# Performance work log

Hardware: AMD Instinct MI355X
Metric: run time of the kernel (lower is better)

Reference implementation:

```python
import jax, jax.numpy as jnp
import numpy as np

B, S, H, NH, HD, I = 2, 1024, 4096, 32, 128, 11008
EPS = 1e-6
THETA = 10000.0


def _rmsnorm(x, w):
    v = jnp.mean(x * x, axis=-1, keepdims=True)
    return x * jax.lax.rsqrt(v + EPS) * w


def _quant(x):
    # per-tensor symmetric int8 quantization (scale already folded upstream)
    return jnp.clip(jnp.round(x), -128.0, 127.0)


def _lin_i8(xq_i8, w_i8, scale, bias):
    acc = jnp.matmul(xq_i8.astype(jnp.int32), w_i8.astype(jnp.int32).T)
    return acc.astype(jnp.float32) * scale + bias


def _rope(q, k):
    pos = jnp.arange(S, dtype=jnp.float32)
    inv = 1.0 / (THETA ** (jnp.arange(0, HD, 2, dtype=jnp.float32) / HD))
    f = pos[:, None] * inv[None, :]              # [S, HD/2]
    emb = jnp.concatenate([f, f], axis=-1)        # [S, HD]
    cos = jnp.cos(emb)[None, None]                # [1,1,S,HD]
    sin = jnp.sin(emb)[None, None]
    def rot(x):
        return jnp.concatenate([-x[..., HD // 2:], x[..., :HD // 2]], axis=-1)
    return q * cos + rot(q) * sin, k * cos + rot(k) * sin


def setup_inputs() -> dict:
    key = jax.random.key(0)
    ks = jax.random.split(key, 30)
    def w8(k, o, i):
        return jax.random.randint(k, (o, i), -128, 128, dtype=jnp.int8)
    def sc(k):
        return jax.random.uniform(k, (), jnp.float32, 0.001, 0.01)
    return {
        "hidden_states": jax.random.normal(ks[0], (B, S, H), jnp.float32),
        "ln1_w": jax.random.uniform(ks[1], (H,), jnp.float32, 0.5, 1.5) * 20.0,
        "ln2_w": jax.random.uniform(ks[2], (H,), jnp.float32, 0.5, 1.5) * 20.0,
        "Wq": w8(ks[3], H, H), "Wk": w8(ks[4], H, H), "Wv": w8(ks[5], H, H),
        "Wo": w8(ks[6], H, H),
        "Wg": w8(ks[7], I, H), "Wu": w8(ks[8], I, H), "Wd": w8(ks[9], H, I),
        "bq": jax.random.normal(ks[10], (H,), jnp.float32) * 0.01,
        "bk": jax.random.normal(ks[11], (H,), jnp.float32) * 0.01,
        "bv": jax.random.normal(ks[12], (H,), jnp.float32) * 0.01,
        "bo": jax.random.normal(ks[13], (H,), jnp.float32) * 0.01,
        "bg": jax.random.normal(ks[14], (I,), jnp.float32) * 0.01,
        "bu": jax.random.normal(ks[15], (I,), jnp.float32) * 0.01,
        "bd": jax.random.normal(ks[16], (H,), jnp.float32) * 0.01,
        "sq": sc(ks[17]) * 1e-3, "sk": sc(ks[18]) * 1e-3, "sv": sc(ks[19]) * 1e-3,
        "so": sc(ks[20]) * 1e-3, "sg": sc(ks[21]) * 1e-3, "su": sc(ks[22]) * 1e-3,
        "sd": sc(ks[23]) * 1e-3,
        "o_in_scale": sc(ks[24]), "down_in_scale": sc(ks[25]),
    }


def reference(hidden_states, ln1_w, ln2_w, Wq, Wk, Wv, Wo, Wg, Wu, Wd,
              bq, bk, bv, bo, bg, bu, bd,
              sq, sk, sv, so, sg, su, sd, o_in_scale, down_in_scale):
    residual = hidden_states
    # input RMSNorm (quant scale folded into ln1_w) -> int8 activation
    hq = _quant(_rmsnorm(hidden_states, ln1_w)).astype(jnp.int8)
    q = _lin_i8(hq, Wq, sq, bq).reshape(B, S, NH, HD).transpose(0, 2, 1, 3)
    k = _lin_i8(hq, Wk, sk, bk).reshape(B, S, NH, HD).transpose(0, 2, 1, 3)
    v = _lin_i8(hq, Wv, sv, bv).reshape(B, S, NH, HD).transpose(0, 2, 1, 3)
    q, k = _rope(q, k)
    scores = jnp.einsum("bhqd,bhkd->bhqk", q, k) / np.float32(np.sqrt(HD))
    causal = jnp.tril(jnp.ones((S, S), dtype=bool))
    scores = jnp.where(causal[None, None], scores, jnp.float32(-1e30))
    attn = jax.nn.softmax(scores, axis=-1)
    o = jnp.einsum("bhqk,bhkd->bhqd", attn, v).transpose(0, 2, 1, 3).reshape(B, S, H)
    # o_proj with quant scale (W8A8BFP32OFP32LinearWithQuantScale)
    oq = _quant(o / o_in_scale).astype(jnp.int8)
    h = residual + _lin_i8(oq, Wo, so, bo)
    residual = h
    # post-attention RMSNorm (fc1 quant scale folded into ln2_w)
    hq2 = _quant(_rmsnorm(h, ln2_w)).astype(jnp.int8)
    g = _lin_i8(hq2, Wg, sg, bg)
    u = _lin_i8(hq2, Wu, su, bu)
    a = jax.nn.silu(g) * u
    aq = _quant(a / down_in_scale).astype(jnp.int8)
    out = residual + _lin_i8(aq, Wd, sd, bd)
    return out
```

## Files before the change

kernel.cpp:

```cpp
#include <hip/hip_runtime.h>
#include <math.h>

#define B_  2
#define S_  1024
#define H_  4096
#define NH_ 32
#define HD_ 128
#define I_  11008
#define R_  2048

typedef __attribute__((ext_vector_type(4))) int i32x4;
typedef __attribute__((ext_vector_type(4))) float f32x4;
typedef __attribute__((ext_vector_type(8))) short bf16x8;


__device__ __forceinline__ void gload_lds16(const void* g, void* l) {
    __builtin_amdgcn_global_load_lds(
        (const __attribute__((address_space(1))) unsigned int*)g,
        (__attribute__((address_space(3))) unsigned int*)l, 16, 0, 0);
}

__device__ __forceinline__ unsigned short f2bf(float f) {
    unsigned int u = __float_as_uint(f);
    u += 0x7fffu + ((u >> 16) & 1u);
    return (unsigned short)(u >> 16);
}

__global__ __launch_bounds__(256)
void packW_k(const int* __restrict__ W, signed char* __restrict__ out, const int K)
{
    const int kt = blockIdx.x, cb = blockIdx.y, nk = gridDim.x;
    const int t = threadIdx.x;
    int* otile = (int*)(out + ((long)(cb * nk + kt) << 13));
#pragma unroll
    for (int i = 0; i < 8; ++i) {
        const int o = i * 256 + t;
        const int g = o >> 9, r = (o >> 2) & 127, jj = o & 3;
        const int4 w4 = *(const int4*)(W + (long)(cb * 128 + r) * K + kt * 64 + g * 16 + jj * 4);
        otile[o] = (w4.x & 255) | ((w4.y & 255) << 8) | ((w4.z & 255) << 16) | (w4.w << 24);
    }
}

__global__ __launch_bounds__(256)
void rmsnorm_quant_k(const float* __restrict__ x, const float* __restrict__ w,
                     signed char* __restrict__ out)
{
    __shared__ float red[4];
    const int tid = threadIdx.x;
    const long row = blockIdx.x;
    const float4* xr = (const float4*)(x + row * H_);
    float4 xv[4];
    float ss = 0.f;
#pragma unroll
    for (int i = 0; i < 4; ++i) {
        xv[i] = xr[tid + i * 256];
        ss += xv[i].x * xv[i].x + xv[i].y * xv[i].y
            + xv[i].z * xv[i].z + xv[i].w * xv[i].w;
    }
#pragma unroll
    for (int off = 32; off; off >>= 1) ss += __shfl_xor(ss, off);
    if ((tid & 63) == 0) red[tid >> 6] = ss;
    __syncthreads();
    const float tot = red[0] + red[1] + red[2] + red[3];
    const float sc = 1.f / sqrtf(tot * (1.f / (float)H_) + 1e-6f);
    const float4* wr = (const float4*)w;
    int* ob = (int*)out;
    const long rb = row >> 7;
    const int rr = (int)(row & 127);
#pragma unroll
    for (int i = 0; i < 4; ++i) {
        const float4 wv = wr[tid + i * 256];
        const int b0 = (int)fminf(fmaxf(rintf(xv[i].x * sc * wv.x), -128.f), 127.f);
        const int b1 = (int)fminf(fmaxf(rintf(xv[i].y * sc * wv.y), -128.f), 127.f);
        const int b2 = (int)fminf(fmaxf(rintf(xv[i].z * sc * wv.z), -128.f), 127.f);
        const int b3 = (int)fminf(fmaxf(rintf(xv[i].w * sc * wv.w), -128.f), 127.f);
        const int packed = (b0 & 255) | ((b1 & 255) << 8) | ((b2 & 255) << 16) | (b3 << 24);
        const int j4 = tid + i * 256;
        const long a32 = ((rb * 64 + (j4 >> 4)) << 11) + (((j4 >> 2) & 3) << 9)
                       + (rr << 2) + (j4 & 3);
        ob[a32] = packed;
    }
}

template<int MODE>
__global__ __launch_bounds__(256, 4)
void gemm_i8t(const signed char* __restrict__ A8, const signed char* __restrict__ W8,
              const float* __restrict__ scale_ptr, const float* __restrict__ bias,
              const float* __restrict__ residual, float* __restrict__ C,
              const float* __restrict__ gbuf, const float* __restrict__ qscale,
              signed char* __restrict__ out8,
              const int N, const int K, const int gx)
{
    __shared__ __align__(16) signed char lsA[2][8192];
    __shared__ __align__(16) signed char lsB[2][8192];

    int bid = blockIdx.x;
    {
        const int nwg = gridDim.x;
        const int q = nwg >> 3, r = nwg & 7;
        const int xcd = bid & 7, idx = bid >> 3;
        bid = (xcd < r) ? (xcd * (q + 1) + idx)
                        : (r * (q + 1) + (xcd - r) * q + idx);
    }
    const int bx = bid % gx, by = bid / gx;

    const int tid  = threadIdx.x;
    const int lane = tid & 63, wid = tid >> 6;
    const int bm = bx << 7, bn = by << 7;
    const int wm = (wid >> 1) << 6, wn = (wid & 1) << 6;

    i32x4 acc[4][4];
#pragma unroll
    for (int m = 0; m < 4; ++m)
#pragma unroll
        for (int n = 0; n < 4; ++n) acc[m][n] = (i32x4){0, 0, 0, 0};

    const int nk = K >> 6;
    const signed char* abase = A8 + ((long)bx * nk << 13);
    const signed char* bbase = W8 + ((long)by * nk << 13);
    const int so0 = wid * 2048 + lane * 16;

    {
        const signed char* at = abase;
        const signed char* bt = bbase;
        gload_lds16(at + so0,        lsA[0] + wid * 2048);
        gload_lds16(at + so0 + 1024, lsA[0] + wid * 2048 + 1024);
        gload_lds16(bt + so0,        lsB[0] + wid * 2048);
        gload_lds16(bt + so0 + 1024, lsB[0] + wid * 2048 + 1024);
    }
    __syncthreads();

    int cur = 0;
    for (int kt = 0; kt < nk; ++kt) {
        const int nxt = cur ^ 1;
        if (kt + 1 < nk) {
            const signed char* at = abase + ((long)(kt + 1) << 13);
            const signed char* bt = bbase + ((long)(kt + 1) << 13);
            gload_lds16(at + so0,        lsA[nxt] + wid * 2048);
            gload_lds16(at + so0 + 1024, lsA[nxt] + wid * 2048 + 1024);
            gload_lds16(bt + so0,        lsB[nxt] + wid * 2048);
            gload_lds16(bt + so0 + 1024, lsB[nxt] + wid * 2048 + 1024);
        }

        const int kg = (lane >> 4) * 2048, fr = (lane & 15) * 16;
        i32x4 af[4], bf[4];
#pragma unroll
        for (int m = 0; m < 4; ++m)
            af[m] = *(const i32x4*)(lsA[cur] + kg + wm * 16 + m * 256 + fr);
#pragma unroll
        for (int n = 0; n < 4; ++n)
            bf[n] = *(const i32x4*)(lsB[cur] + kg + wn * 16 + n * 256 + fr);
#pragma unroll
        for (int m = 0; m < 4; ++m)
#pragma unroll
            for (int n = 0; n < 4; ++n)
                acc[m][n] = __builtin_amdgcn_mfma_i32_16x16x64_i8(af[m], bf[n], acc[m][n], 0, 0, 0);

        __syncthreads();
        cur = nxt;
    }

    const float s = *scale_ptr;
    const int rq = (lane >> 4) * 4, fc = lane & 15;
    if (MODE == 0) {
#pragma unroll
        for (int m = 0; m < 4; ++m) {
#pragma unroll
            for (int n = 0; n < 4; ++n) {
                const int col = bn + wn + n * 16 + fc;
                const float bcol = bias[col];
#pragma unroll
                for (int r = 0; r < 4; ++r) {
                    const int row = bm + wm + m * 16 + rq + r;
                    float v = (float)acc[m][n][r] * s + bcol;
                    if (residual) v += residual[(long)row * N + col];
                    C[(long)row * N + col] = v;
                }
            }
        }
    } else {
        const float dinv = 1.f / qscale[0];
        const int nko = N >> 6;
#pragma unroll
        for (int m = 0; m < 4; ++m) {
#pragma unroll
            for (int n = 0; n < 4; ++n) {
                const int col = bn + wn + n * 16 + fc;
                const float bcol = bias[col];
                const int ktc = col >> 6, kgc = (col >> 4) & 3, jc = col & 15;
#pragma unroll
                for (int r = 0; r < 4; ++r) {
                    const int row = bm + wm + m * 16 + rq + r;
                    const float u = (float)acc[m][n][r] * s + bcol;
                    const float g = gbuf[(long)row * N + col];
                    const float a = g / (1.f + __expf(-g)) * u;
                    const float qv = fminf(fmaxf(rintf(a * dinv), -128.f), 127.f);
                    const long addr = (((long)(row >> 7) * nko + ktc) << 13)
                                    + (kgc << 11) + ((row & 127) << 4) + jc;
                    out8[addr] = (signed char)(int)qv;
                }
            }
        }
    }
}

__global__ __launch_bounds__(256)
void rope_k(float* __restrict__ q, float* __restrict__ k)
{
    const int row = blockIdx.x;
    const int s = row & (S_ - 1);
    float* qr = q + (long)row * H_;
    float* kr = k + (long)row * H_;
    for (int t = threadIdx.x; t < NH_ * 64; t += 256) {
        const int nh = t >> 6, i = t & 63;
        const float inv = powf(10000.f, -(float)(2 * i) * (1.f / 128.f));
        const float f = (float)s * inv;
        float sn, c;
        sincosf(f, &sn, &c);
        const int base = nh * 128 + i;
        const float q0 = qr[base], q1 = qr[base + 64];
        qr[base]      = q0 * c - q1 * sn;
        qr[base + 64] = q1 * c + q0 * sn;
        const float k0 = kr[base], k1 = kr[base + 64];
        kr[base]      = k0 * c - k1 * sn;
        kr[base + 64] = k1 * c + k0 * sn;
    }
}

__global__ __launch_bounds__(256, 2)
void attn_mfma_k(const float* __restrict__ q, const float* __restrict__ k,
                 const float* __restrict__ v, signed char* __restrict__ out8,
                 const float* __restrict__ osc)
{
    __shared__ __align__(16) char lsK[8192];
    __shared__ __align__(16) char lsV[10240];
    __shared__ __align__(16) char lsP[4][1024];

    const int tid = threadIdx.x, lane = tid & 63, wid = tid >> 6;
    const int bid = blockIdx.x;
    const int qt = 15 - (bid >> 6);
    const int bh = bid & 63;
    const int b = bh >> 5, h = bh & 31;
    const int q0 = qt * 64;
    const int qw = q0 + wid * 16;

    const float* qbase = q + (long)(b * S_) * H_ + (long)h * HD_;
    const float* kbase = k + (long)(b * S_) * H_ + (long)h * HD_;
    const float* vbase = v + (long)(b * S_) * H_ + (long)h * HD_;

    const int frow = lane & 15, fgrp = lane >> 4;
    const float sc = 0.08838834764831845f;

    bf16x8 qf[4];
    {
        const float* qr = qbase + (long)(qw + frow) * H_;
#pragma unroll
        for (int c = 0; c < 4; ++c) {
            const float4 a = *(const float4*)(qr + c * 32 + fgrp * 8);
            const float4 bq = *(const float4*)(qr + c * 32 + fgrp * 8 + 4);
            bf16x8 t;
            t[0] = (short)f2bf(a.x * sc);  t[1] = (short)f2bf(a.y * sc);
            t[2] = (short)f2bf(a.z * sc);  t[3] = (short)f2bf(a.w * sc);
            t[4] = (short)f2bf(bq.x * sc); t[5] = (short)f2bf(bq.y * sc);
            t[6] = (short)f2bf(bq.z * sc); t[7] = (short)f2bf(bq.w * sc);
            qf[c] = t;
        }
    }

    f32x4 oacc[8];
#pragma unroll
    for (int n2 = 0; n2 < 8; ++n2) oacc[n2] = (f32x4){0.f, 0.f, 0.f, 0.f};
    float mr[4] = {-1e30f, -1e30f, -1e30f, -1e30f};
    float lr[4] = {0.f, 0.f, 0.f, 0.f};

    const int nt = (q0 >> 5) + 2;
    for (int kt = 0; kt < nt; ++kt) {
        if (kt) __syncthreads();
        {
            const float* kg = kbase + (long)(kt * 32) * H_;
            const float* vg = vbase + (long)(kt * 32) * H_;
#pragma unroll
            for (int i = 0; i < 4; ++i) {
                const int lin = i * 256 + tid;
                const int kr = lin >> 5;
                const int d4 = (lin & 31) * 4;
                const float4 kv = *(const float4*)(kg + (long)kr * H_ + d4);
                const float4 vv = *(const float4*)(vg + (long)kr * H_ + d4);
                ushort4 kb;
                kb.x = f2bf(kv.x); kb.y = f2bf(kv.y); kb.z = f2bf(kv.z); kb.w = f2bf(kv.w);
                *(ushort4*)(lsK + kr * 256 + ((d4 * 2) ^ ((kr & 7) << 4))) = kb;
                *(unsigned short*)(lsV + (d4 + 0) * 80 + kr * 2) = f2bf(vv.x);
                *(unsigned short*)(lsV + (d4 + 1) * 80 + kr * 2) = f2bf(vv.y);
                *(unsigned short*)(lsV + (d4 + 2) * 80 + kr * 2) = f2bf(vv.z);
                *(unsigned short*)(lsV + (d4 + 3) * 80 + kr * 2) = f2bf(vv.w);
            }
        }
        __syncthreads();

        if (kt * 32 <= qw + 15) {
            f32x4 s0 = (f32x4){0.f, 0.f, 0.f, 0.f};
            f32x4 s1 = (f32x4){0.f, 0.f, 0.f, 0.f};
            const int swz = (frow & 7) << 4;
#pragma unroll
            for (int c = 0; c < 4; ++c) {
                const int dby = c * 64 + fgrp * 16;
                const bf16x8 kfA = *(const bf16x8*)(lsK + frow * 256 + (dby ^ swz));
                const bf16x8 kfB = *(const bf16x8*)(lsK + (frow + 16) * 256 + (dby ^ swz));
                s0 = __builtin_amdgcn_mfma_f32_16x16x32_bf16(qf[c], kfA, s0, 0, 0, 0);
                s1 = __builtin_amdgcn_mfma_f32_16x16x32_bf16(qf[c], kfB, s1, 0, 0, 0);
            }

            const int colg0 = kt * 32 + frow;
            float cf[4];
#pragma unroll
            for (int r = 0; r < 4; ++r) {
                const int rowg = qw + fgrp * 4 + r;
                const float a0 = (colg0 <= rowg) ? s0[r] : -1e30f;
                const float a1 = (colg0 + 16 <= rowg) ? s1[r] : -1e30f;
                float mx = fmaxf(a0, a1);
#pragma unroll
                for (int off2 = 1; off2 < 16; off2 <<= 1) mx = fmaxf(mx, __shfl_xor(mx, off2));
                const float mnew = fmaxf(mr[r], mx);
                cf[r] = __expf(mr[r] - mnew);
                mr[r] = mnew;
                const float p0 = __expf(a0 - mnew);
                const float p1 = __expf(a1 - mnew);
                float sm = p0 + p1;
#pragma unroll
                for (int off2 = 1; off2 < 16; off2 <<= 1) sm += __shfl_xor(sm, off2);
                lr[r] = lr[r] * cf[r] + sm;
                const int row = fgrp * 4 + r;
                const int psw = (row & 3) << 4;
                *(unsigned short*)(lsP[wid] + row * 64 + ((frow * 2) ^ psw)) = f2bf(p0);
                *(unsigned short*)(lsP[wid] + row * 64 + (((16 + frow) * 2) ^ psw)) = f2bf(p1);
            }
#pragma unroll
            for (int n2 = 0; n2 < 8; ++n2) {
#pragma unroll
                for (int r = 0; r < 4; ++r) oacc[n2][r] *= cf[r];
            }
            const bf16x8 pf = *(const bf16x8*)(lsP[wid] + frow * 64 + ((fgrp * 16) ^ ((frow & 3) << 4)));
#pragma unroll
            for (int n2 = 0; n2 < 8; ++n2) {
                const bf16x8 vf = *(const bf16x8*)(lsV + (n2 * 16 + frow) * 80 + fgrp * 16);
                oacc[n2] = __builtin_amdgcn_mfma_f32_16x16x32_bf16(pf, vf, oacc[n2], 0, 0, 0);
            }
        }
    }

    const float oinv = 1.f / osc[0];
    float inv[4];
#pragma unroll
    for (int r = 0; r < 4; ++r) inv[r] = 1.f / lr[r];
#pragma unroll
    for (int n2 = 0; n2 < 8; ++n2) {
        const int kk = h * 128 + n2 * 16 + frow;
        const int ktc = kk >> 6, kgc = (kk >> 4) & 3, jc = kk & 15;
#pragma unroll
        for (int r = 0; r < 4; ++r) {
            const int rowt = b * S_ + qw + fgrp * 4 + r;
            const float ov = oacc[n2][r] * inv[r];
            const float qv = fminf(fmaxf(rintf(ov * oinv), -128.f), 127.f);
            const long addr = (((long)(rowt >> 7) * 64 + ktc) << 13)
                            + (kgc << 11) + ((rowt & 127) << 4) + jc;
            out8[addr] = (signed char)(int)qv;
        }
    }
}

extern "C" void kernel_launch(void* const* d_in, const int* in_sizes, int n_in,
                              void* d_out, int out_size, void* d_ws, size_t ws_size,
                              hipStream_t stream)
{
    const float* hidden = (const float*)d_in[0];
    const float* ln1 = (const float*)d_in[1];
    const float* ln2 = (const float*)d_in[2];
    const int* Wq = (const int*)d_in[3];
    const int* Wk = (const int*)d_in[4];
    const int* Wv = (const int*)d_in[5];
    const int* Wo = (const int*)d_in[6];
    const int* Wg = (const int*)d_in[7];
    const int* Wu = (const int*)d_in[8];
    const int* Wd = (const int*)d_in[9];
    const float* bq = (const float*)d_in[10];
    const float* bk = (const float*)d_in[11];
    const float* bv = (const float*)d_in[12];
    const float* bo = (const float*)d_in[13];
    const float* bg = (const float*)d_in[14];
    const float* bu = (const float*)d_in[15];
    const float* bd = (const float*)d_in[16];
    const float* sq = (const float*)d_in[17];
    const float* sk = (const float*)d_in[18];
    const float* sv = (const float*)d_in[19];
    const float* so = (const float*)d_in[20];
    const float* sg = (const float*)d_in[21];
    const float* su = (const float*)d_in[22];
    const float* sd = (const float*)d_in[23];
    const float* o_sc = (const float*)d_in[24];
    const float* d_sc = (const float*)d_in[25];

    char* ws = (char*)d_ws;
    signed char* HQ8 = (signed char*)ws;
    signed char* WP  = (signed char*)(ws + ((size_t)22 << 20));
    float* Qb = (float*)(ws + ((size_t)66 << 20));
    float* Kb = (float*)(ws + ((size_t)98 << 20));
    float* Vb = (float*)(ws + ((size_t)130 << 20));
    float* Gb = (float*)(ws + ((size_t)98 << 20));
    signed char* AQ8 = (signed char*)(ws + ((size_t)184 << 20));
    float* Hb = Qb;
    float* out = (float*)d_out;

    const dim3 blk(256);
    const int gxH = R_ / 128;
    const int nwgH = gxH * (H_ / 128);
    const int nwgI = gxH * (I_ / 128);
    const dim3 gpH(H_ / 64, H_ / 128);
    const dim3 gpI(H_ / 64, I_ / 128);
    const dim3 gpD(I_ / 64, H_ / 128);

    rmsnorm_quant_k<<<R_, blk, 0, stream>>>(hidden, ln1, HQ8);

    packW_k<<<gpH, blk, 0, stream>>>(Wq, WP, H_);
    gemm_i8t<0><<<nwgH, blk, 0, stream>>>(HQ8, WP, sq, bq, nullptr, Qb,
                                          nullptr, nullptr, nullptr, H_, H_, gxH);
    packW_k<<<gpH, blk, 0, stream>>>(Wk, WP, H_);
    gemm_i8t<0><<<nwgH, blk, 0, stream>>>(HQ8, WP, sk, bk, nullptr, Kb,
                                          nullptr, nullptr, nullptr, H_, H_, gxH);
    packW_k<<<gpH, blk, 0, stream>>>(Wv, WP, H_);
    gemm_i8t<0><<<nwgH, blk, 0, stream>>>(HQ8, WP, sv, bv, nullptr, Vb,
                                          nullptr, nullptr, nullptr, H_, H_, gxH);

    rope_k<<<R_, blk, 0, stream>>>(Qb, Kb);
    attn_mfma_k<<<B_ * NH_ * (S_ / 64), blk, 0, stream>>>(Qb, Kb, Vb, HQ8, o_sc);

    packW_k<<<gpH, blk, 0, stream>>>(Wo, WP, H_);
    gemm_i8t<0><<<nwgH, blk, 0, stream>>>(HQ8, WP, so, bo, hidden, Hb,
                                          nullptr, nullptr, nullptr, H_, H_, gxH);

    rmsnorm_quant_k<<<R_, blk, 0, stream>>>(Hb, ln2, HQ8);

    packW_k<<<gpI, blk, 0, stream>>>(Wg, WP, H_);
    gemm_i8t<0><<<nwgI, blk, 0, stream>>>(HQ8, WP, sg, bg, nullptr, Gb,
                                          nullptr, nullptr, nullptr, I_, H_, gxH);
    packW_k<<<gpI, blk, 0, stream>>>(Wu, WP, H_);
    gemm_i8t<1><<<nwgI, blk, 0, stream>>>(HQ8, WP, su, bu, nullptr, nullptr,
                                          Gb, d_sc, AQ8, I_, H_, gxH);
    packW_k<<<gpD, blk, 0, stream>>>(Wd, WP, I_);
    gemm_i8t<0><<<nwgH, blk, 0, stream>>>(AQ8, WP, sd, bd, Hb, out,
                                          nullptr, nullptr, nullptr, H_, I_, gxH);
}
```

Measured before the change: 1.004 ms.

## Triple-buffer int8 GEMM LDS tiles with explicit vmcnt waits and MFMA priority

```diff
diff --git a/kernel.cpp b/kernel.cpp
--- a/kernel.cpp
+++ b/kernel.cpp
@@ -83,7 +83,7 @@
 }
 
 template<int MODE>
-__global__ __launch_bounds__(256, 4)
+__global__ __launch_bounds__(256, 3)
 void gemm_i8t(const signed char* __restrict__ A8, const signed char* __restrict__ W8,
               const float* __restrict__ scale_ptr, const float* __restrict__ bias,
               const float* __restrict__ residual, float* __restrict__ C,
@@ -91,8 +91,8 @@
               signed char* __restrict__ out8,
               const int N, const int K, const int gx)
 {
-    __shared__ __align__(16) signed char lsA[2][8192];
-    __shared__ __align__(16) signed char lsB[2][8192];
+    __shared__ __align__(16) signed char lsA[3][8192];
+    __shared__ __align__(16) signed char lsB[3][8192];
 
     int bid = blockIdx.x;
     {
@@ -119,28 +119,33 @@
     const signed char* abase = A8 + ((long)bx * nk << 13);
     const signed char* bbase = W8 + ((long)by * nk << 13);
     const int so0 = wid * 2048 + lane * 16;
-
-    {
-        const signed char* at = abase;
-        const signed char* bt = bbase;
-        gload_lds16(at + so0,        lsA[0] + wid * 2048);
-        gload_lds16(at + so0 + 1024, lsA[0] + wid * 2048 + 1024);
-        gload_lds16(bt + so0,        lsB[0] + wid * 2048);
-        gload_lds16(bt + so0 + 1024, lsB[0] + wid * 2048 + 1024);
-    }
-    __syncthreads();
-
-    int cur = 0;
+    const int ld0 = wid * 2048;
+
+#pragma unroll
+    for (int t = 0; t < 2; ++t) {
+        const signed char* at = abase + ((long)t << 13);
+        const signed char* bt = bbase + ((long)t << 13);
+        gload_lds16(at + so0,        lsA[t] + ld0);
+        gload_lds16(at + so0 + 1024, lsA[t] + ld0 + 1024);
+        gload_lds16(bt + so0,        lsB[t] + ld0);
+        gload_lds16(bt + so0 + 1024, lsB[t] + ld0 + 1024);
+    }
+
     for (int kt = 0; kt < nk; ++kt) {
-        const int nxt = cur ^ 1;
-        if (kt + 1 < nk) {
-            const signed char* at = abase + ((long)(kt + 1) << 13);
-            const signed char* bt = bbase + ((long)(kt + 1) << 13);
-            gload_lds16(at + so0,        lsA[nxt] + wid * 2048);
-            gload_lds16(at + so0 + 1024, lsA[nxt] + wid * 2048 + 1024);
-            gload_lds16(bt + so0,        lsB[nxt] + wid * 2048);
-            gload_lds16(bt + so0 + 1024, lsB[nxt] + wid * 2048 + 1024);
-        }
+        const int cur = kt % 3;
+        if (kt + 2 < nk) {
+            const int pb = (kt + 2) % 3;
+            const signed char* at = abase + ((long)(kt + 2) << 13);
+            const signed char* bt = bbase + ((long)(kt + 2) << 13);
+            gload_lds16(at + so0,        lsA[pb] + ld0);
+            gload_lds16(at + so0 + 1024, lsA[pb] + ld0 + 1024);
+            gload_lds16(bt + so0,        lsB[pb] + ld0);
+            gload_lds16(bt + so0 + 1024, lsB[pb] + ld0 + 1024);
+        }
+        if (kt + 2 < nk)      asm volatile("s_waitcnt vmcnt(8)" ::: "memory");
+        else if (kt + 1 < nk) asm volatile("s_waitcnt vmcnt(4)" ::: "memory");
+        else                  asm volatile("s_waitcnt vmcnt(0)" ::: "memory");
+        __builtin_amdgcn_s_barrier();
 
         const int kg = (lane >> 4) * 2048, fr = (lane & 15) * 16;
         i32x4 af[4], bf[4];
@@ -150,14 +155,14 @@
 #pragma unroll
         for (int n = 0; n < 4; ++n)
             bf[n] = *(const i32x4*)(lsB[cur] + kg + wn * 16 + n * 256 + fr);
+        __builtin_amdgcn_s_setprio(1);
 #pragma unroll
         for (int m = 0; m < 4; ++m)
 #pragma unroll
             for (int n = 0; n < 4; ++n)
                 acc[m][n] = __builtin_amdgcn_mfma_i32_16x16x64_i8(af[m], bf[n], acc[m][n], 0, 0, 0);
-
-        __syncthreads();
-        cur = nxt;
+        __builtin_amdgcn_s_setprio(0);
+        __builtin_amdgcn_s_barrier();
     }
 
     const float s = *scale_ptr;
```

Measured after the change: 997.1 us. About the same (-0.7%).
